# Kernel optimization log

Measured on AMD Instinct MI355X. Metric: run time of the kernel, lower is better.

## Reference

```python
import jax, jax.numpy as jnp
import numpy as np
import math

N_HEADS = 8
INPUT_DIM = 512
EMBED_DIM = 512
KEY_DIM = EMBED_DIM // N_HEADS  # 64, also val_dim
BATCH = 16
GRAPH = 1024


def setup_inputs() -> dict:
    key = jax.random.key(0)
    ks = jax.random.split(key, 10)
    def uinit(k, shape):
        stdv = 1.0 / math.sqrt(shape[-1])
        return jax.random.uniform(k, shape, jnp.float32, -stdv, stdv)
    return {
        "h_node_in": jax.random.normal(ks[0], (BATCH, GRAPH, INPUT_DIM), jnp.float32),
        "h_pos_in": jax.random.normal(ks[1], (BATCH, GRAPH, INPUT_DIM), jnp.float32),
        "W_query_node": uinit(ks[2], (N_HEADS, INPUT_DIM, KEY_DIM)),
        "W_query_pos": uinit(ks[3], (N_HEADS, INPUT_DIM, KEY_DIM)),
        "W_key_node": uinit(ks[4], (N_HEADS, INPUT_DIM, KEY_DIM)),
        "W_key_pos": uinit(ks[5], (N_HEADS, INPUT_DIM, KEY_DIM)),
        "W_val_node": uinit(ks[6], (2 * N_HEADS, INPUT_DIM, KEY_DIM)),
        "W_val_pos": uinit(ks[7], (2 * N_HEADS, INPUT_DIM, KEY_DIM)),
        "W_out_node": uinit(ks[8], (N_HEADS, 2 * KEY_DIM, EMBED_DIM)),
        "W_out_pos": uinit(ks[9], (N_HEADS, 2 * KEY_DIM, EMBED_DIM)),
    }


def reference(h_node_in, h_pos_in, W_query_node, W_query_pos, W_key_node,
              W_key_pos, W_val_node, W_val_pos, W_out_node, W_out_pos):
    norm = 1.0 / math.sqrt(KEY_DIM)
    H = N_HEADS
    # projections: [B,N,D] x [H,D,k] -> [H,B,N,k]
    Q_node = jnp.einsum('bnd,hdk->hbnk', h_node_in, W_query_node)
    Q_pos = jnp.einsum('bnd,hdk->hbnk', h_pos_in, W_query_pos)
    K_node = jnp.einsum('bnd,hdk->hbnk', h_node_in, W_key_node)
    K_pos = jnp.einsum('bnd,hdk->hbnk', h_pos_in, W_key_pos)
    # values: [2H,D,v] -> (2,H,B,N,v)
    V_node = jnp.einsum('bnd,hdv->hbnv', h_node_in, W_val_node).reshape(2, H, *h_node_in.shape[:2], KEY_DIM)
    V_pos = jnp.einsum('bnd,hdv->hbnv', h_pos_in, W_val_pos).reshape(2, H, *h_pos_in.shape[:2], KEY_DIM)
    # two shared softmax attentions: [H,B,Nq,Nk]
    attn1 = jax.nn.softmax(norm * jnp.einsum('hbqk,hbnk->hbqn', Q_node, K_node), axis=-1)
    attn2 = jax.nn.softmax(norm * jnp.einsum('hbqk,hbnk->hbqn', Q_pos, K_pos), axis=-1)
    heads_node = jnp.concatenate([
        jnp.einsum('hbqn,hbnv->hbqv', attn1, V_node[0]),
        jnp.einsum('hbqn,hbnv->hbqv', attn2, V_node[1])], axis=-1)  # [H,B,N,2v]
    heads_pos = jnp.concatenate([
        jnp.einsum('hbqn,hbnv->hbqv', attn1, V_pos[0]),
        jnp.einsum('hbqn,hbnv->hbqv', attn2, V_pos[1])], axis=-1)
    # per-head output GEMM, summed over heads: [H,B,N,2v] x [H,2v,E] -> [B,N,E]
    out_node = jnp.einsum('hbnc,hce->bne', heads_node, W_out_node)
    out_pos = jnp.einsum('hbnc,hce->bne', heads_pos, W_out_pos)
    return (out_node, out_pos)
```

## Files before the change

kernel.cpp:

```cpp
#include <hip/hip_runtime.h>
#include <hip/hip_bf16.h>
#include <stdint.h>

typedef __attribute__((ext_vector_type(8))) short short8;
typedef __attribute__((ext_vector_type(4))) short short4_t;
typedef __attribute__((ext_vector_type(4))) float f32x4;
typedef __attribute__((ext_vector_type(16))) float f32x16;
typedef __attribute__((ext_vector_type(4))) unsigned uint4v;

#define DEVFN static __device__ __forceinline__

constexpr int BATCH = 16;
constexpr int GRAPH = 1024;
constexpr int IDIM  = 512;
constexpr int EDIM  = 512;
constexpr int NH    = 8;
constexpr int KD    = 64;
constexpr int TOK   = BATCH * GRAPH;
constexpr int QKC   = 1024;
constexpr int HC    = 1024;
constexpr float SMSCALE = 0.125f * 1.44269504088896340736f;

DEVFN unsigned short f2bf(float x) {
    union { float f; unsigned u; } v; v.f = x;
    unsigned r = v.u + 0x7fffu + ((v.u >> 16) & 1u);
    return (unsigned short)(r >> 16);
}

DEVFN unsigned cvtpk(float a, float b) {
    unsigned r;
    asm("v_cvt_pk_bf16_f32 %0, %1, %2" : "=v"(r) : "v"(a), "v"(b));
    return r;
}

DEVFN void plswap(unsigned &x, unsigned &y) {
    asm("v_permlane32_swap_b32 %0, %1" : "+v"(x), "+v"(y));
}

DEVFN void load16(const void* g, void* l) {
    __builtin_amdgcn_global_load_lds(
        (const __attribute__((address_space(1))) void*)g,
        (__attribute__((address_space(3))) void*)l, 16, 0, 0);
}

__global__ __launch_bounds__(256) void cvt_x_kernel(const float4* __restrict__ x0,
                                                    const float4* __restrict__ x1,
                                                    short4_t* __restrict__ y0,
                                                    short4_t* __restrict__ y1) {
    const float4* x = blockIdx.y ? x1 : x0;
    short4_t*     y = blockIdx.y ? y1 : y0;
    const int i = blockIdx.x * 256 + threadIdx.x;
    const float4 v = x[i];
    short4_t o;
    o[0] = (short)f2bf(v.x); o[1] = (short)f2bf(v.y);
    o[2] = (short)f2bf(v.z); o[3] = (short)f2bf(v.w);
    y[i] = o;
}

__global__ __launch_bounds__(256) void pack_qkv_kernel(const float* __restrict__ Wq0,
                                                       const float* __restrict__ Wk0,
                                                       const float* __restrict__ Wv0,
                                                       const float* __restrict__ Wq1,
                                                       const float* __restrict__ Wk1,
                                                       const float* __restrict__ Wv1,
                                                       unsigned short* __restrict__ Wp0,
                                                       unsigned short* __restrict__ Wp1) {
    const float* Wq = blockIdx.y ? Wq1 : Wq0;
    const float* Wk = blockIdx.y ? Wk1 : Wk0;
    const float* Wv = blockIdx.y ? Wv1 : Wv0;
    unsigned short* Wp = blockIdx.y ? Wp1 : Wp0;
    const int idx = blockIdx.x * 256 + threadIdx.x;
    const int col = idx >> 9, d = idx & 511;
    float v;
    if (col < 512)       v = Wq[((col >> 6) * IDIM + d) * KD + (col & 63)] * SMSCALE;
    else if (col < 1024) v = Wk[(((col - 512) >> 6) * IDIM + d) * KD + (col & 63)];
    else                 v = Wv[(((col - 1024) >> 6) * IDIM + d) * KD + (col & 63)];
    Wp[idx] = f2bf(v);
}

__global__ __launch_bounds__(256) void pack_out_kernel(const float* __restrict__ W0,
                                                       const float* __restrict__ W1,
                                                       unsigned short* __restrict__ Wp0,
                                                       unsigned short* __restrict__ Wp1) {
    const float* W = blockIdx.y ? W1 : W0;
    unsigned short* Wp = blockIdx.y ? Wp1 : Wp0;
    const int idx = blockIdx.x * 256 + threadIdx.x;
    const int e = idx >> 10, c = idx & 1023;
    Wp[idx] = f2bf(W[(size_t)c * EDIM + e]);
}

template<int K, bool VSPLIT, typename OutT>
__global__ __launch_bounds__(256)
void gemm_bt_kernel(const unsigned short* __restrict__ A0, const unsigned short* __restrict__ A1,
                    const unsigned short* __restrict__ B0, const unsigned short* __restrict__ B1,
                    OutT* __restrict__ C0, OutT* __restrict__ C1,
                    unsigned short* __restrict__ V0, unsigned short* __restrict__ V1,
                    int ldc)
{
    __shared__ unsigned short As[128 * 64];
    __shared__ unsigned short Bs[128 * 64];
    const unsigned short* A  = blockIdx.z ? A1 : A0;
    const unsigned short* Bt = blockIdx.z ? B1 : B0;

    const int tid = threadIdx.x, wave = tid >> 6, lane = tid & 63;
    const int g = lane >> 4, ln = lane & 15;
    const int m0 = blockIdx.x * 128, n0 = blockIdx.y * 128;
    const int wr = (wave >> 1) * 64, wc = (wave & 1) * 64;

    f32x4 acc[4][4] = {};

    for (int k0 = 0; k0 < K; k0 += 64) {
        #pragma unroll
        for (int j = 0; j < 4; ++j) {
            const int c = (wave * 4 + j) * 64 + lane;
            const int row = c >> 3;
            const int col = ((c & 7) ^ (row & 7)) * 8;
            load16(A  + (size_t)(m0 + row) * K + k0 + col, (char*)As + c * 16);
            load16(Bt + (size_t)(n0 + row) * K + k0 + col, (char*)Bs + c * 16);
        }
        __syncthreads();
        #pragma unroll
        for (int kk = 0; kk < 2; ++kk) {
            short8 af[4], bfr[4];
            #pragma unroll
            for (int i = 0; i < 4; ++i) {
                const int ra = wr + i * 16 + ln;
                af[i]  = *(const short8*)((const char*)As + ra * 128 + (((kk * 4 + g) ^ (ra & 7)) * 16));
                const int rb = wc + i * 16 + ln;
                bfr[i] = *(const short8*)((const char*)Bs + rb * 128 + (((kk * 4 + g) ^ (rb & 7)) * 16));
            }
            #pragma unroll
            for (int mi = 0; mi < 4; ++mi)
                #pragma unroll
                for (int ni = 0; ni < 4; ++ni)
                    acc[mi][ni] = __builtin_amdgcn_mfma_f32_16x16x32_bf16(af[mi], bfr[ni], acc[mi][ni], 0, 0, 0);
        }
        __syncthreads();
    }

    if (!VSPLIT || n0 < 1024) {
        OutT* C = blockIdx.z ? C1 : C0;
        #pragma unroll
        for (int mi = 0; mi < 4; ++mi)
            #pragma unroll
            for (int ni = 0; ni < 4; ++ni)
                #pragma unroll
                for (int r = 0; r < 4; ++r) {
                    const size_t m = (size_t)(m0 + wr + mi * 16 + g * 4 + r);
                    const size_t n = (size_t)(n0 + wc + ni * 16 + ln);
                    if constexpr (sizeof(OutT) == 4) C[m * ldc + n] = acc[mi][ni][r];
                    else                             C[m * ldc + n] = (OutT)f2bf(acc[mi][ni][r]);
                }
    } else {
        unsigned short* Vt = blockIdx.z ? V1 : V0;
        #pragma unroll
        for (int mi = 0; mi < 4; ++mi)
            #pragma unroll
            for (int ni = 0; ni < 4; ++ni) {
                uint2 w;
                w.x = cvtpk(acc[mi][ni][0], acc[mi][ni][1]);
                w.y = cvtpk(acc[mi][ni][2], acc[mi][ni][3]);
                const size_t vrow = (size_t)(n0 - 1024 + wc + ni * 16 + ln);
                const size_t mcol = (size_t)(m0 + wr + mi * 16 + g * 4);
                *(uint2*)(Vt + vrow * TOK + mcol) = w;
            }
    }
}

__global__ __launch_bounds__(256, 3)
void attn_kernel(const unsigned short* __restrict__ projn,
                 const unsigned short* __restrict__ projp,
                 const unsigned short* __restrict__ Vtn,
                 const unsigned short* __restrict__ Vtp,
                 unsigned short* __restrict__ headsn,
                 unsigned short* __restrict__ headsp)
{
    __shared__ unsigned short Kl[2][64 * 64];
    __shared__ unsigned short Vl[2][128 * 64];

    const int qt = blockIdx.x;
    const int a  = blockIdx.y >> 3, h = blockIdx.y & 7;
    const int b  = blockIdx.z;
    const int tid = threadIdx.x, wave = tid >> 6, lane = tid & 63;
    const int q = lane & 31, hi = lane >> 5;

    const unsigned short* proj = a ? projp : projn;
    const int tok0 = b * GRAPH;
    const size_t qrow = (size_t)(tok0 + qt * 128 + wave * 32 + q);
    const int qc  = h * KD;
    const int kc  = IDIM + h * KD;
    const int vr0 = (a * NH + h) * KD;

    short8 qf[4];
    #pragma unroll
    for (int ds = 0; ds < 4; ++ds)
        qf[ds] = *(const short8*)(proj + qrow * QKC + qc + ds * 16 + hi * 8);

    const char* kap[2]; int kds[2];
    #pragma unroll
    for (int j = 0; j < 2; ++j) {
        const int c = (wave * 2 + j) * 64 + lane;
        const int row = c >> 3;
        const int col = ((c & 7) ^ (row & 7)) * 8;
        kap[j] = (const char*)(proj + (size_t)(tok0 + row) * QKC + kc + col);
        kds[j] = c * 16;
    }
    const char* vap[4]; int vds[4];
    #pragma unroll
    for (int j = 0; j < 4; ++j) {
        const int c = (wave * 4 + j) * 64 + lane;
        const int row = c >> 3;
        const int col = ((c & 7) ^ (row & 7)) * 8;
        const unsigned short* base = (row < 64)
            ? (Vtn + (size_t)(vr0 + row) * TOK)
            : (Vtp + (size_t)(vr0 + row - 64) * TOK);
        vap[j] = (const char*)(base + tok0 + col);
        vds[j] = c * 16;
    }

    auto stage = [&](int bb) {
        #pragma unroll
        for (int j = 0; j < 2; ++j) { load16(kap[j], (char*)Kl[bb] + kds[j]); kap[j] += (size_t)64 * QKC * 2; }
        #pragma unroll
        for (int j = 0; j < 4; ++j) { load16(vap[j], (char*)Vl[bb] + vds[j]); vap[j] += 64 * 2; }
    };

    f32x16 oacc[4] = {};
    float l_run = 0.f;

    stage(0);
    __syncthreads();

    for (int kt = 0; kt < 16; ++kt) {
        const int bb = kt & 1;
        if (kt < 15) stage(bb ^ 1);

        f32x16 sacc[2] = {};
        __builtin_amdgcn_s_setprio(1);
        #pragma unroll
        for (int ds = 0; ds < 4; ++ds) {
            #pragma unroll
            for (int kb = 0; kb < 2; ++kb) {
                const int row = kb * 32 + q;
                const short8 kf = *(const short8*)((const char*)Kl[bb] + row * 128 + (((ds * 2 + hi) ^ (row & 7)) * 16));
                sacc[kb] = __builtin_amdgcn_mfma_f32_32x32x16_bf16(kf, qf[ds], sacc[kb], 0, 0, 0);
            }
        }
        __builtin_amdgcn_s_setprio(0);

        float psum = 0.f;
        #pragma unroll
        for (int kb = 0; kb < 2; ++kb)
            #pragma unroll
            for (int r = 0; r < 16; ++r) {
                const float pv = __builtin_amdgcn_exp2f(sacc[kb][r]);
                sacc[kb][r] = pv;
                psum += pv;
            }
        psum += __shfl_xor(psum, 32);
        l_run += psum;

        short8 pfrag[4];
        #pragma unroll
        for (int s = 0; s < 4; ++s) {
            const int kb = s >> 1, o = 4 * (s & 1);
            unsigned A0 = cvtpk(sacc[kb][2 * o + 0], sacc[kb][2 * o + 1]);
            unsigned A1 = cvtpk(sacc[kb][2 * o + 2], sacc[kb][2 * o + 3]);
            unsigned B0 = cvtpk(sacc[kb][2 * o + 4], sacc[kb][2 * o + 5]);
            unsigned B1 = cvtpk(sacc[kb][2 * o + 6], sacc[kb][2 * o + 7]);
            plswap(A0, B0);
            plswap(A1, B1);
            uint4v pw; pw[0] = A0; pw[1] = A1; pw[2] = B0; pw[3] = B1;
            pfrag[s] = __builtin_bit_cast(short8, pw);
        }

        __builtin_amdgcn_s_setprio(1);
        #pragma unroll
        for (int s = 0; s < 4; ++s) {
            #pragma unroll
            for (int vb = 0; vb < 4; ++vb) {
                const int row = vb * 32 + q;
                const short8 vf = *(const short8*)((const char*)Vl[bb] + row * 128 + (((s * 2 + hi) ^ (row & 7)) * 16));
                oacc[vb] = __builtin_amdgcn_mfma_f32_32x32x16_bf16(vf, pfrag[s], oacc[vb], 0, 0, 0);
            }
        }
        __builtin_amdgcn_s_setprio(0);
        __syncthreads();
    }

    const float inv = 1.0f / l_run;
    #pragma unroll
    for (int vb = 0; vb < 4; ++vb) {
        unsigned short* heads = (vb < 2) ? headsn : headsp;
        const int colbase = h * 128 + a * 64 + (vb & 1) * 32;
        #pragma unroll
        for (int w = 0; w < 8; ++w) {
            const unsigned pk = cvtpk(oacc[vb][2 * w] * inv, oacc[vb][2 * w + 1] * inv);
            const int v = ((2 * w) & 3) + 8 * (w >> 1) + 4 * hi;
            *(unsigned*)(heads + qrow * HC + colbase + v) = pk;
        }
    }
}

extern "C" void kernel_launch(void* const* d_in, const int* in_sizes, int n_in,
                              void* d_out, int out_size, void* d_ws, size_t ws_size,
                              hipStream_t stream)
{
    const float* hn  = (const float*)d_in[0];
    const float* hp  = (const float*)d_in[1];
    const float* Wqn = (const float*)d_in[2];
    const float* Wqp = (const float*)d_in[3];
    const float* Wkn = (const float*)d_in[4];
    const float* Wkp = (const float*)d_in[5];
    const float* Wvn = (const float*)d_in[6];
    const float* Wvp = (const float*)d_in[7];
    const float* Won = (const float*)d_in[8];
    const float* Wop = (const float*)d_in[9];
    float* out = (float*)d_out;

    char* ws = (char*)d_ws;
    size_t off = 0;
    auto take = [&](size_t nbytes) -> char* {
        char* p = ws + off;
        off += (nbytes + 255) & ~(size_t)255;
        return p;
    };
    unsigned short* Xn  = (unsigned short*)take((size_t)TOK * IDIM * 2);
    unsigned short* Xp  = (unsigned short*)take((size_t)TOK * IDIM * 2);
    unsigned short* Wn  = (unsigned short*)take((size_t)2048 * 512 * 2);
    unsigned short* Wp  = (unsigned short*)take((size_t)2048 * 512 * 2);
    unsigned short* WoN = (unsigned short*)take((size_t)512 * 1024 * 2);
    unsigned short* WoP = (unsigned short*)take((size_t)512 * 1024 * 2);
    unsigned short* Pn  = (unsigned short*)take((size_t)TOK * QKC * 2);
    unsigned short* Pp  = (unsigned short*)take((size_t)TOK * QKC * 2);
    unsigned short* Vtn = (unsigned short*)take((size_t)1024 * TOK * 2);
    unsigned short* Vtp = (unsigned short*)take((size_t)1024 * TOK * 2);
    unsigned short* Hn  = (unsigned short*)take((size_t)TOK * HC * 2);
    unsigned short* Hp  = (unsigned short*)take((size_t)TOK * HC * 2);

    cvt_x_kernel<<<dim3(TOK * IDIM / 4 / 256, 2), 256, 0, stream>>>(
        (const float4*)hn, (const float4*)hp, (short4_t*)Xn, (short4_t*)Xp);
    pack_qkv_kernel<<<dim3(2048 * 512 / 256, 2), 256, 0, stream>>>(
        Wqn, Wkn, Wvn, Wqp, Wkp, Wvp, Wn, Wp);
    pack_out_kernel<<<dim3(512 * 1024 / 256, 2), 256, 0, stream>>>(Won, Wop, WoN, WoP);

    gemm_bt_kernel<512, true, unsigned short><<<dim3(128, 16, 2), 256, 0, stream>>>(
        Xn, Xp, Wn, Wp, Pn, Pp, Vtn, Vtp, QKC);

    attn_kernel<<<dim3(8, 16, 16), 256, 0, stream>>>(Pn, Pp, Vtn, Vtp, Hn, Hp);

    gemm_bt_kernel<1024, false, float><<<dim3(128, 4, 2), 256, 0, stream>>>(
        Hn, Hp, WoN, WoP, out, out + (size_t)TOK * EDIM,
        (unsigned short*)nullptr, (unsigned short*)nullptr, EDIM);
}
```

Before: 445.4 us.

## Double per-wave query rows in attention, swizzle grid, fuse weight packing

The attention kernel now has each wave handle 64 query rows (two 32-row MFMA tiles), so every K and V fragment read from LDS feeds two MFMAs. This halves K/V LDS and global staging traffic per query, at the cost of more accumulator registers, so the occupancy hint drops from 3 to 2 blocks. The grid is flattened to a 1D launch and remapped so blocks sharing a (batch, head) group are spread across XCD-interleaved IDs, which is meant to improve L2 locality. The two weight-packing kernels are merged into one launch that transposes through an LDS tile, so both global reads and writes are coalesced.

```diff
diff --git a/kernel.cpp b/kernel.cpp
--- a/kernel.cpp
+++ b/kernel.cpp
@@ -57,36 +57,61 @@
     y[i] = o;
 }
 
-__global__ __launch_bounds__(256) void pack_qkv_kernel(const float* __restrict__ Wq0,
-                                                       const float* __restrict__ Wk0,
-                                                       const float* __restrict__ Wv0,
-                                                       const float* __restrict__ Wq1,
-                                                       const float* __restrict__ Wk1,
-                                                       const float* __restrict__ Wv1,
-                                                       unsigned short* __restrict__ Wp0,
-                                                       unsigned short* __restrict__ Wp1) {
-    const float* Wq = blockIdx.y ? Wq1 : Wq0;
-    const float* Wk = blockIdx.y ? Wk1 : Wk0;
-    const float* Wv = blockIdx.y ? Wv1 : Wv0;
-    unsigned short* Wp = blockIdx.y ? Wp1 : Wp0;
-    const int idx = blockIdx.x * 256 + threadIdx.x;
-    const int col = idx >> 9, d = idx & 511;
-    float v;
-    if (col < 512)       v = Wq[((col >> 6) * IDIM + d) * KD + (col & 63)] * SMSCALE;
-    else if (col < 1024) v = Wk[(((col - 512) >> 6) * IDIM + d) * KD + (col & 63)];
-    else                 v = Wv[(((col - 1024) >> 6) * IDIM + d) * KD + (col & 63)];
-    Wp[idx] = f2bf(v);
-}
-
-__global__ __launch_bounds__(256) void pack_out_kernel(const float* __restrict__ W0,
-                                                       const float* __restrict__ W1,
-                                                       unsigned short* __restrict__ Wp0,
-                                                       unsigned short* __restrict__ Wp1) {
-    const float* W = blockIdx.y ? W1 : W0;
-    unsigned short* Wp = blockIdx.y ? Wp1 : Wp0;
-    const int idx = blockIdx.x * 256 + threadIdx.x;
-    const int e = idx >> 10, c = idx & 1023;
-    Wp[idx] = f2bf(W[(size_t)c * EDIM + e]);
+__global__ __launch_bounds__(256)
+void pack_w_kernel(const float* __restrict__ Wqn, const float* __restrict__ Wkn,
+                   const float* __restrict__ Wvn,
+                   const float* __restrict__ Wqp, const float* __restrict__ Wkp,
+                   const float* __restrict__ Wvp,
+                   const float* __restrict__ Won, const float* __restrict__ Wop,
+                   unsigned short* __restrict__ Wn, unsigned short* __restrict__ Wp2,
+                   unsigned short* __restrict__ WoN, unsigned short* __restrict__ WoP)
+{
+    __shared__ float T[64][65];
+    const int bid = blockIdx.x, tid = threadIdx.x;
+
+    const float* src; unsigned short* dst;
+    int sld, dld; size_t sbase, dbase;
+    float scale = 1.f;
+
+    if (bid < 512) {
+        const int st = bid >> 8, t = bid & 255;
+        const int tr = t >> 3, tc = t & 7;
+        dst = st ? Wp2 : Wn;
+        int head;
+        if (tr < 8)       { src = st ? Wqp : Wqn; head = tr;      scale = SMSCALE; }
+        else if (tr < 16) { src = st ? Wkp : Wkn; head = tr - 8; }
+        else              { src = st ? Wvp : Wvn; head = tr - 16; }
+        sld = 64; dld = 512;
+        sbase = (size_t)(head * 512 + tc * 64) * 64;
+        dbase = (size_t)(tr * 64) * 512 + tc * 64;
+    } else {
+        const int b2 = bid - 512;
+        const int st = b2 >> 7, t = b2 & 127;
+        const int tr = t >> 4, tc = t & 15;
+        src = st ? Wop : Won;
+        dst = st ? WoP : WoN;
+        sld = 512; dld = 1024;
+        sbase = (size_t)(tc * 64) * 512 + tr * 64;
+        dbase = (size_t)(tr * 64) * 1024 + tc * 64;
+    }
+
+    {
+        const int j = tid & 63, i0 = tid >> 6;
+        #pragma unroll
+        for (int p = 0; p < 16; ++p) {
+            const int i = p * 4 + i0;
+            T[i][j] = src[sbase + (size_t)i * sld + j];
+        }
+    }
+    __syncthreads();
+    {
+        const int i = tid & 63, j0 = tid >> 6;
+        #pragma unroll
+        for (int p = 0; p < 16; ++p) {
+            const int j = p * 4 + j0;
+            dst[dbase + (size_t)j * dld + i] = f2bf(T[i][j] * scale);
+        }
+    }
 }
 
 template<int K, bool VSPLIT, typename OutT>
@@ -167,7 +192,7 @@
     }
 }
 
-__global__ __launch_bounds__(256, 3)
+__global__ __launch_bounds__(256, 2)
 void attn_kernel(const unsigned short* __restrict__ projn,
                  const unsigned short* __restrict__ projp,
                  const unsigned short* __restrict__ Vtn,
@@ -178,23 +203,29 @@
     __shared__ unsigned short Kl[2][64 * 64];
     __shared__ unsigned short Vl[2][128 * 64];
 
-    const int qt = blockIdx.x;
-    const int a  = blockIdx.y >> 3, h = blockIdx.y & 7;
-    const int b  = blockIdx.z;
+    const int bid  = blockIdx.x;
+    const int slot = bid >> 3;
+    const int g    = (bid & 7) * 32 + (slot >> 2);
+    const int qt   = slot & 3;
+    const int a    = (g & 15) >> 3, h = g & 7;
+    const int b    = g >> 4;
+
     const int tid = threadIdx.x, wave = tid >> 6, lane = tid & 63;
     const int q = lane & 31, hi = lane >> 5;
 
     const unsigned short* proj = a ? projp : projn;
     const int tok0 = b * GRAPH;
-    const size_t qrow = (size_t)(tok0 + qt * 128 + wave * 32 + q);
+    const size_t qrow0 = (size_t)(tok0 + qt * 256 + wave * 64 + q);
     const int qc  = h * KD;
     const int kc  = IDIM + h * KD;
     const int vr0 = (a * NH + h) * KD;
 
-    short8 qf[4];
+    short8 qf[2][4];
     #pragma unroll
-    for (int ds = 0; ds < 4; ++ds)
-        qf[ds] = *(const short8*)(proj + qrow * QKC + qc + ds * 16 + hi * 8);
+    for (int qi = 0; qi < 2; ++qi)
+        #pragma unroll
+        for (int ds = 0; ds < 4; ++ds)
+            qf[qi][ds] = *(const short8*)(proj + (qrow0 + qi * 32) * QKC + qc + ds * 16 + hi * 8);
 
     const char* kap[2]; int kds[2];
     #pragma unroll
@@ -225,8 +256,8 @@
         for (int j = 0; j < 4; ++j) { load16(vap[j], (char*)Vl[bb] + vds[j]); vap[j] += 64 * 2; }
     };
 
-    f32x16 oacc[4] = {};
-    float l_run = 0.f;
+    f32x16 oacc[2][4] = {};
+    float l_run[2] = {0.f, 0.f};
 
     stage(0);
     __syncthreads();
@@ -235,43 +266,50 @@
         const int bb = kt & 1;
         if (kt < 15) stage(bb ^ 1);
 
-        f32x16 sacc[2] = {};
-        __builtin_amdgcn_s_setprio(1);
-        #pragma unroll
-        for (int ds = 0; ds < 4; ++ds) {
-            #pragma unroll
-            for (int kb = 0; kb < 2; ++kb) {
+        short8 pfrag[2][4];
+        #pragma unroll
+        for (int kb = 0; kb < 2; ++kb) {
+            f32x16 s0 = {}, s1 = {};
+            __builtin_amdgcn_s_setprio(1);
+            #pragma unroll
+            for (int ds = 0; ds < 4; ++ds) {
                 const int row = kb * 32 + q;
                 const short8 kf = *(const short8*)((const char*)Kl[bb] + row * 128 + (((ds * 2 + hi) ^ (row & 7)) * 16));
-                sacc[kb] = __builtin_amdgcn_mfma_f32_32x32x16_bf16(kf, qf[ds], sacc[kb], 0, 0, 0);
-            }
-        }
-        __builtin_amdgcn_s_setprio(0);
-
-        float psum = 0.f;
-        #pragma unroll
-        for (int kb = 0; kb < 2; ++kb)
+                s0 = __builtin_amdgcn_mfma_f32_32x32x16_bf16(kf, qf[0][ds], s0, 0, 0, 0);
+                s1 = __builtin_amdgcn_mfma_f32_32x32x16_bf16(kf, qf[1][ds], s1, 0, 0, 0);
+            }
+            __builtin_amdgcn_s_setprio(0);
+
+            float ps0 = 0.f, ps1 = 0.f;
             #pragma unroll
             for (int r = 0; r < 16; ++r) {
-                const float pv = __builtin_amdgcn_exp2f(sacc[kb][r]);
-                sacc[kb][r] = pv;
-                psum += pv;
-            }
-        psum += __shfl_xor(psum, 32);
-        l_run += psum;
-
-        short8 pfrag[4];
-        #pragma unroll
-        for (int s = 0; s < 4; ++s) {
-            const int kb = s >> 1, o = 4 * (s & 1);
-            unsigned A0 = cvtpk(sacc[kb][2 * o + 0], sacc[kb][2 * o + 1]);
-            unsigned A1 = cvtpk(sacc[kb][2 * o + 2], sacc[kb][2 * o + 3]);
-            unsigned B0 = cvtpk(sacc[kb][2 * o + 4], sacc[kb][2 * o + 5]);
-            unsigned B1 = cvtpk(sacc[kb][2 * o + 6], sacc[kb][2 * o + 7]);
-            plswap(A0, B0);
-            plswap(A1, B1);
-            uint4v pw; pw[0] = A0; pw[1] = A1; pw[2] = B0; pw[3] = B1;
-            pfrag[s] = __builtin_bit_cast(short8, pw);
+                const float p0 = __builtin_amdgcn_exp2f(s0[r]); s0[r] = p0; ps0 += p0;
+                const float p1 = __builtin_amdgcn_exp2f(s1[r]); s1[r] = p1; ps1 += p1;
+            }
+            l_run[0] += ps0; l_run[1] += ps1;
+
+            #pragma unroll
+            for (int sh = 0; sh < 2; ++sh) {
+                const int s = kb * 2 + sh, o = 8 * sh;
+                {
+                    unsigned A0 = cvtpk(s0[o + 0], s0[o + 1]);
+                    unsigned A1 = cvtpk(s0[o + 2], s0[o + 3]);
+                    unsigned B0 = cvtpk(s0[o + 4], s0[o + 5]);
+                    unsigned B1 = cvtpk(s0[o + 6], s0[o + 7]);
+                    plswap(A0, B0); plswap(A1, B1);
+                    uint4v pw; pw[0] = A0; pw[1] = A1; pw[2] = B0; pw[3] = B1;
+                    pfrag[0][s] = __builtin_bit_cast(short8, pw);
+                }
+                {
+                    unsigned A0 = cvtpk(s1[o + 0], s1[o + 1]);
+                    unsigned A1 = cvtpk(s1[o + 2], s1[o + 3]);
+                    unsigned B0 = cvtpk(s1[o + 4], s1[o + 5]);
+                    unsigned B1 = cvtpk(s1[o + 6], s1[o + 7]);
+                    plswap(A0, B0); plswap(A1, B1);
+                    uint4v pw; pw[0] = A0; pw[1] = A1; pw[2] = B0; pw[3] = B1;
+                    pfrag[1][s] = __builtin_bit_cast(short8, pw);
+                }
+            }
         }
 
         __builtin_amdgcn_s_setprio(1);
@@ -281,23 +319,29 @@
             for (int vb = 0; vb < 4; ++vb) {
                 const int row = vb * 32 + q;
                 const short8 vf = *(const short8*)((const char*)Vl[bb] + row * 128 + (((s * 2 + hi) ^ (row & 7)) * 16));
-                oacc[vb] = __builtin_amdgcn_mfma_f32_32x32x16_bf16(vf, pfrag[s], oacc[vb], 0, 0, 0);
+                oacc[0][vb] = __builtin_amdgcn_mfma_f32_32x32x16_bf16(vf, pfrag[0][s], oacc[0][vb], 0, 0, 0);
+                oacc[1][vb] = __builtin_amdgcn_mfma_f32_32x32x16_bf16(vf, pfrag[1][s], oacc[1][vb], 0, 0, 0);
             }
         }
         __builtin_amdgcn_s_setprio(0);
         __syncthreads();
     }
 
-    const float inv = 1.0f / l_run;
     #pragma unroll
-    for (int vb = 0; vb < 4; ++vb) {
-        unsigned short* heads = (vb < 2) ? headsn : headsp;
-        const int colbase = h * 128 + a * 64 + (vb & 1) * 32;
-        #pragma unroll
-        for (int w = 0; w < 8; ++w) {
-            const unsigned pk = cvtpk(oacc[vb][2 * w] * inv, oacc[vb][2 * w + 1] * inv);
-            const int v = ((2 * w) & 3) + 8 * (w >> 1) + 4 * hi;
-            *(unsigned*)(heads + qrow * HC + colbase + v) = pk;
+    for (int qi = 0; qi < 2; ++qi) {
+        l_run[qi] += __shfl_xor(l_run[qi], 32);
+        const float inv = 1.0f / l_run[qi];
+        const size_t qrow = qrow0 + qi * 32;
+        #pragma unroll
+        for (int vb = 0; vb < 4; ++vb) {
+            unsigned short* heads = (vb < 2) ? headsn : headsp;
+            const int colbase = h * 128 + a * 64 + (vb & 1) * 32;
+            #pragma unroll
+            for (int w = 0; w < 8; ++w) {
+                const unsigned pk = cvtpk(oacc[qi][vb][2 * w] * inv, oacc[qi][vb][2 * w + 1] * inv);
+                const int v = ((2 * w) & 3) + 8 * (w >> 1) + 4 * hi;
+                *(unsigned*)(heads + qrow * HC + colbase + v) = pk;
+            }
         }
     }
 }
@@ -340,14 +384,13 @@
 
     cvt_x_kernel<<<dim3(TOK * IDIM / 4 / 256, 2), 256, 0, stream>>>(
         (const float4*)hn, (const float4*)hp, (short4_t*)Xn, (short4_t*)Xp);
-    pack_qkv_kernel<<<dim3(2048 * 512 / 256, 2), 256, 0, stream>>>(
-        Wqn, Wkn, Wvn, Wqp, Wkp, Wvp, Wn, Wp);
-    pack_out_kernel<<<dim3(512 * 1024 / 256, 2), 256, 0, stream>>>(Won, Wop, WoN, WoP);
+    pack_w_kernel<<<768, 256, 0, stream>>>(
+        Wqn, Wkn, Wvn, Wqp, Wkp, Wvp, Won, Wop, Wn, Wp, WoN, WoP);
 
     gemm_bt_kernel<512, true, unsigned short><<<dim3(128, 16, 2), 256, 0, stream>>>(
         Xn, Xp, Wn, Wp, Pn, Pp, Vtn, Vtp, QKC);
 
-    attn_kernel<<<dim3(8, 16, 16), 256, 0, stream>>>(Pn, Pp, Vtn, Vtp, Hn, Hp);
+    attn_kernel<<<1024, 256, 0, stream>>>(Pn, Pp, Vtn, Vtp, Hn, Hp);
 
     gemm_bt_kernel<1024, false, float><<<dim3(128, 4, 2), 256, 0, stream>>>(
         Hn, Hp, WoN, WoP, out, out + (size_t)TOK * EDIM,
```

Result: faster. 405.5 us (-9.0%).
